# Kernel optimization log

Hardware: AMD Instinct MI355X
Metric: run time of the kernel (lower is better)

## Reference

```python
import jax, jax.numpy as jnp
import numpy as np

N_NODES = 100_000
N_EDGES = 1_600_000
D_FEAT = 128
D_HID = 128
D_OUT = 1


def _w(key, fan_in, fan_out):
    # PyG Linear default (glorot-ish); exact init irrelevant for a math reference
    return jax.random.normal(key, (fan_in, fan_out), dtype=jnp.float32) * (1.0 / np.sqrt(fan_in))


def setup_inputs() -> dict:
    key = jax.random.key(0)
    ks = jax.random.split(key, 20)
    inp = {
        "x": jax.random.normal(ks[0], (N_NODES, D_FEAT), dtype=jnp.float32),
        "edge_index": jax.random.randint(ks[1], (2, N_EDGES), 0, N_NODES, dtype=jnp.int32),
    }
    dims = [(D_FEAT, D_HID), (D_HID, D_HID), (D_HID, D_OUT)]
    i = 2
    for li, (din, dout) in enumerate(dims, start=1):
        inp[f"Wk{li}"] = _w(ks[i + 0], din, dout)
        inp[f"Wq{li}"] = _w(ks[i + 1], din, dout)
        inp[f"Wv{li}"] = _w(ks[i + 2], din, dout)
        inp[f"Ws{li}"] = _w(ks[i + 3], din, dout)
        inp[f"b{li}"] = jnp.zeros((dout,), dtype=jnp.float32)
        i += 4
    return inp


def _res_gated_conv(x, src, dst, Wk, Wq, Wv, Ws, b):
    # out_i = Ws x_i + b + sum_{j->i} sigmoid(Wk x_i + Wq x_j) * (Wv x_j)
    k = x @ Wk          # [N, Dout] (keyed by target)
    q = x @ Wq          # [N, Dout] (keyed by source)
    v = x @ Wv          # [N, Dout]
    eta = jax.nn.sigmoid(k[dst] + q[src])          # [E, Dout] edge gate
    msg = eta * v[src]                             # [E, Dout]
    agg = jax.ops.segment_sum(msg, dst, num_segments=x.shape[0])  # scatter-add
    return agg + x @ Ws + b


def reference(x, edge_index, Wk1, Wq1, Wv1, Ws1, b1, Wk2, Wq2, Wv2, Ws2, b2,
              Wk3, Wq3, Wv3, Ws3, b3):
    src = edge_index[0]
    dst = edge_index[1]
    x = jax.nn.relu(_res_gated_conv(x, src, dst, Wk1, Wq1, Wv1, Ws1, b1))
    x = jax.nn.relu(_res_gated_conv(x, src, dst, Wk2, Wq2, Wv2, Ws2, b2))
    return _res_gated_conv(x, src, dst, Wk3, Wq3, Wv3, Ws3, b3)  # [N, 1]
```

## Files before the change

kernel.cpp:

```cpp
#include <hip/hip_runtime.h>
#include <hip/hip_bf16.h>
#include <cstdint>

typedef unsigned short u16;
typedef unsigned int   u32;
typedef __attribute__((ext_vector_type(8))) short bf16x8;
typedef __attribute__((ext_vector_type(4))) float f32x4;

#define NEG_LOG2E -1.44269504088896f

__device__ __forceinline__ float bf2f(u16 u) {
    union { u32 i; float f; } c; c.i = ((u32)u) << 16; return c.f;
}
__device__ __forceinline__ u16 f2bf(float f) {
    union { float f; u32 i; } c; c.f = f;
    u32 x = c.i;
    return (u16)((x + 0x7fffu + ((x >> 16) & 1u)) >> 16);
}
__device__ __forceinline__ void bfu2(u32 p, float& lo, float& hi) {
    union { u32 i; float f; } a, b;
    a.i = p << 16; b.i = p & 0xffff0000u;
    lo = a.f; hi = b.f;
}
__device__ __forceinline__ float gate(float zt) {
    return __builtin_amdgcn_rcpf(1.0f + __builtin_amdgcn_exp2f(zt));
}

struct P8 { const float* p[8]; };
__global__ __launch_bounds__(256)
void prep_k(P8 wsrc, u16* __restrict__ Wt) {
    int t = threadIdx.x;
    int mat = blockIdx.x >> 3, seg = blockIdx.x & 7;
    const float* W = wsrc.p[mat];
    u16* T = Wt + (size_t)mat * 16384;
    for (int p = 0; p < 8; ++p) {
        int idx = seg * 2048 + p * 256 + t;
        int k = idx >> 7, n = idx & 127;
        T[n * 128 + k] = f2bf(W[k * 128 + n]);
    }
}


#define CSR_CH 2048

__global__ __launch_bounds__(256)
void sortA_hist(const int* __restrict__ dst, int* __restrict__ cnt,
                int nE, int NA, int nbuck) {
    __shared__ int lh[512];
    int t = threadIdx.x, b = blockIdx.x;
    for (int i = t; i < nbuck; i += 256) lh[i] = 0;
    __syncthreads();
    int i0 = b * CSR_CH, iend = min(i0 + CSR_CH, nE);
    for (int i = i0 + t; i < iend; i += 256) atomicAdd(&lh[dst[i] >> 8], 1);
    __syncthreads();
    for (int i = t; i < nbuck; i += 256) cnt[i * NA + b] = lh[i];
}

__global__ __launch_bounds__(256)
void scan_part_k(const int* __restrict__ arr, int* __restrict__ part, int M) {
    __shared__ int wsum[4];
    int t = threadIdx.x, lane = t & 63, wave = t >> 6;
    int i0 = blockIdx.x * 1024 + t * 4;
    int s = 0;
    for (int j = 0; j < 4; ++j) { int i = i0 + j; if (i < M) s += arr[i]; }
    for (int off = 32; off > 0; off >>= 1) s += __shfl_xor(s, off);
    if (lane == 0) wsum[wave] = s;
    __syncthreads();
    if (t == 0) part[blockIdx.x] = wsum[0] + wsum[1] + wsum[2] + wsum[3];
}

__global__ __launch_bounds__(512)
void scan_tops512(int* __restrict__ part, int nb) {
    __shared__ int sh[512];
    int t = threadIdx.x;
    int v = (t < nb) ? part[t] : 0;
    sh[t] = v;
    __syncthreads();
    for (int off = 1; off < 512; off <<= 1) {
        int u = (t >= off) ? sh[t - off] : 0;
        __syncthreads();
        sh[t] += u;
        __syncthreads();
    }
    if (t < nb) part[t] = sh[t] - v;
}

__global__ __launch_bounds__(256)
void scan_emit_k(const int* __restrict__ arr, const int* __restrict__ part,
                 int* __restrict__ outp, int M, int total) {
    __shared__ int woff[4];
    int t = threadIdx.x, lane = t & 63, wave = t >> 6;
    int i0 = blockIdx.x * 1024 + t * 4;
    int d[4]; int s = 0;
    for (int j = 0; j < 4; ++j) { int i = i0 + j; d[j] = (i < M) ? arr[i] : 0; s += d[j]; }
    int ws = s;
    for (int off = 1; off < 64; off <<= 1) {
        int u = __shfl_up(ws, off);
        if (lane >= off) ws += u;
    }
    if (lane == 63) woff[wave] = ws;
    __syncthreads();
    int base = part[blockIdx.x];
    for (int w = 0; w < wave; ++w) base += woff[w];
    int ex = base + ws - s;
    for (int j = 0; j < 4; ++j) {
        int i = i0 + j;
        if (i < M) outp[i] = ex;
        ex += d[j];
    }
    if (blockIdx.x == 0 && t == 0) outp[M] = total;
}

__global__ __launch_bounds__(256)
void sortA_scat(const int* __restrict__ src, const int* __restrict__ dst,
                const int* __restrict__ scnt, u32* __restrict__ tkey,
                int nE, int NA, int nbuck) {
    __shared__ int lh[512];
    __shared__ int lbase[512];
    int t = threadIdx.x, b = blockIdx.x;
    for (int i = t; i < nbuck; i += 256) { lh[i] = 0; lbase[i] = scnt[i * NA + b]; }
    __syncthreads();
    int i0 = b * CSR_CH, iend = min(i0 + CSR_CH, nE);
    for (int i = i0 + t; i < iend; i += 256) {
        int d = dst[i], s = src[i];
        int bk = d >> 8;
        int r = atomicAdd(&lh[bk], 1);
        tkey[lbase[bk] + r] = ((u32)(d & 255) << 24) | (u32)s;
    }
}

__global__ __launch_bounds__(256)
void sortB(const u32* __restrict__ tkey, const int* __restrict__ scnt,
           int* __restrict__ rowp, int* __restrict__ ssrc,
           int NA, int N, int nE) {
    __shared__ int h[256];
    __shared__ int off[256];
    int t = threadIdx.x, b = blockIdx.x;
    int base = scnt[b * NA];
    int endp = scnt[(b + 1) * NA];
    h[t] = 0;
    __syncthreads();
    for (int i = base + t; i < endp; i += 256)
        atomicAdd(&h[tkey[i] >> 24], 1);
    __syncthreads();
    int v = h[t];
    off[t] = v;
    __syncthreads();
    for (int d = 1; d < 256; d <<= 1) {
        int u = (t >= d) ? off[t - d] : 0;
        __syncthreads();
        off[t] += u;
        __syncthreads();
    }
    int ex = off[t] - v;
    __syncthreads();
    off[t] = ex;
    h[t] = 0;
    __syncthreads();
    int dglob = b * 256 + t;
    if (dglob < N) rowp[dglob] = base + ex;
    if (b == 0 && t == 0) rowp[N] = nE;
    for (int i = base + t; i < endp; i += 256) {
        u32 k = tkey[i];
        int loc = k >> 24;
        int r = atomicAdd(&h[loc], 1);
        ssrc[base + off[loc] + r] = (int)(k & 0xFFFFFFu);
    }
}

#define XS 136
template<int F32>
__global__ __launch_bounds__(256, 2)
void gemm_kqvs(const void* __restrict__ Xv, const u16* __restrict__ Wt,
               const float* __restrict__ bias,
               u16* __restrict__ KS, u16* __restrict__ QV, int nrows)
{
    __shared__ u16 xs[128 * XS];
    __shared__ u16 wsl[128 * XS];
    const int tid  = threadIdx.x;
    const int wave = tid >> 6, lane = tid & 63;
    const int quad = lane >> 4, l16 = lane & 15;
    const int r0 = blockIdx.x * 128;

    for (int p = 0; p < 8; ++p) {
        int c = p * 256 + tid;
        int row = c >> 4;
        int col = (c & 15) * 8;
        int gr = r0 + row; if (gr >= nrows) gr = nrows - 1;
        if (F32) {
            const float* sp = (const float*)Xv + (size_t)gr * 128 + col;
            float4 f0 = *(const float4*)(sp);
            float4 f1 = *(const float4*)(sp + 4);
            uint4 st;
            st.x = ((u32)f2bf(f0.y) << 16) | f2bf(f0.x);
            st.y = ((u32)f2bf(f0.w) << 16) | f2bf(f0.z);
            st.z = ((u32)f2bf(f1.y) << 16) | f2bf(f1.x);
            st.w = ((u32)f2bf(f1.w) << 16) | f2bf(f1.z);
            *(uint4*)(&xs[row * XS + col]) = st;
        } else {
            uint4 d = *(const uint4*)((const u16*)Xv + (size_t)gr * 128 + col);
            *(uint4*)(&xs[row * XS + col]) = d;
        }
    }

    for (int wi = 0; wi < 4; ++wi) {
        __syncthreads();
        const u16* Wsrc = Wt + wi * (128 * 128);
        for (int p = 0; p < 8; ++p) {
            int c = p * 256 + tid;
            int row = c >> 4;
            int col = (c & 15) * 8;
            uint4 d = *(const uint4*)(Wsrc + row * 128 + col);
            *(uint4*)(&wsl[row * XS + col]) = d;
        }
        __syncthreads();

        f32x4 acc[2][8];
        for (int mt = 0; mt < 2; ++mt)
            for (int nt = 0; nt < 8; ++nt) acc[mt][nt] = (f32x4)0.0f;

        const int cbase = wave * 32;
        for (int kt = 0; kt < 4; ++kt) {
            bf16x8 a0 = *(const bf16x8*)&wsl[(cbase + l16)      * XS + kt * 32 + quad * 8];
            bf16x8 a1 = *(const bf16x8*)&wsl[(cbase + 16 + l16) * XS + kt * 32 + quad * 8];
            for (int nt = 0; nt < 8; ++nt) {
                bf16x8 b = *(const bf16x8*)&xs[(nt * 16 + l16) * XS + kt * 32 + quad * 8];
                acc[0][nt] = __builtin_amdgcn_mfma_f32_16x16x32_bf16(a0, b, acc[0][nt], 0, 0, 0);
                acc[1][nt] = __builtin_amdgcn_mfma_f32_16x16x32_bf16(a1, b, acc[1][nt], 0, 0, 0);
            }
        }

        float4 bias4[2];
        if (wi == 3) {
            bias4[0] = *(const float4*)(bias + cbase + quad * 4);
            bias4[1] = *(const float4*)(bias + cbase + 16 + quad * 4);
        }
        for (int mt = 0; mt < 2; ++mt) {
            int chb = cbase + mt * 16 + quad * 4;
            for (int nt = 0; nt < 8; ++nt) {
                int node = r0 + nt * 16 + l16;
                if (node >= nrows) continue;
                f32x4 v = acc[mt][nt];
                float x0 = v[0], x1 = v[1], x2 = v[2], x3 = v[3];
                if (wi == 0 || wi == 1) {
                    x0 *= NEG_LOG2E; x1 *= NEG_LOG2E; x2 *= NEG_LOG2E; x3 *= NEG_LOG2E;
                } else if (wi == 3) {
                    x0 += bias4[mt].x; x1 += bias4[mt].y;
                    x2 += bias4[mt].z; x3 += bias4[mt].w;
                }
                uint2 st;
                st.x = ((u32)f2bf(x1) << 16) | f2bf(x0);
                st.y = ((u32)f2bf(x3) << 16) | f2bf(x2);
                size_t nb = (size_t)node * 256;
                if      (wi == 0) *(uint2*)(KS + nb + chb) = st;
                else if (wi == 3) *(uint2*)(KS + nb + 128 + chb) = st;
                else if (wi == 1) *(uint2*)(QV + nb + 2 * chb) = st;
                else              *(uint2*)(QV + nb + 2 * chb + 4) = st;
            }
        }
    }
}

template<int MODE>
__global__ __launch_bounds__(256)
void edge_csr2(const int* __restrict__ rowp, const int* __restrict__ ssrc,
               const u16* __restrict__ KS, const u16* __restrict__ QV,
               u16* __restrict__ Xout,
               const float* __restrict__ Wk3, const float* __restrict__ Wq3,
               const float* __restrict__ Wv3, const float* __restrict__ Ws3,
               const float* __restrict__ b3,
               float* __restrict__ k3, float2* __restrict__ qv3,
               float* __restrict__ s3, int N)
{
    const int lane = threadIdx.x & 63;
    const int half = lane >> 5;
    const int t    = lane & 31;
    int gw = blockIdx.x * (blockDim.x >> 6) + (threadIdx.x >> 6);
    int nw = gridDim.x * (blockDim.x >> 6);

    float4 wk4, wq4, wv4, ws4;
    float bias3 = 0.0f;
    if (MODE == 1) {
        wk4 = *(const float4*)(Wk3 + 4 * t);
        wq4 = *(const float4*)(Wq3 + 4 * t);
        wv4 = *(const float4*)(Wv3 + 4 * t);
        ws4 = *(const float4*)(Ws3 + 4 * t);
        bias3 = b3[0];
    }

#define LOAD2(S0, S1) (*((const uint4*)(QV + (size_t)(half ? (S1) : (S0)) * 256) + t))
#define COMP(QVv, A0, A1, A2, A3)                                             \
    {                                                                         \
        float q0_, q1_, q2_, q3_, v0_, v1_, v2_, v3_;                         \
        bfu2((QVv).x, q0_, q1_); bfu2((QVv).y, q2_, q3_);                     \
        bfu2((QVv).z, v0_, v1_); bfu2((QVv).w, v2_, v3_);                     \
        A0 += gate(k0 + q0_) * v0_;  A1 += gate(k1 + q1_) * v1_;              \
        A2 += gate(k2 + q2_) * v2_;  A3 += gate(k3v + q3_) * v3_;             \
    }

    for (int d = gw; d < N; d += nw) {
        int beg = rowp[d], end = rowp[d + 1];
        uint2 kk = *(const uint2*)(KS + (size_t)d * 256 + t * 4);
        float k0, k1, k2, k3v;
        bfu2(kk.x, k0, k1); bfu2(kk.y, k2, k3v);
        float a0 = 0.f, a1 = 0.f, a2 = 0.f, a3 = 0.f;
        float e0 = 0.f, e1 = 0.f, e2 = 0.f, e3 = 0.f;

        for (int base = beg; base < end; base += 64) {
            int e = base + lane;
            int sv = (e < end) ? ssrc[e] : 0;
            int m = end - base; if (m > 64) m = 64;
            int j = 0;
            for (; j + 4 <= m; j += 4) {
                int sa0 = __builtin_amdgcn_readlane(sv, j);
                int sa1 = __builtin_amdgcn_readlane(sv, j + 1);
                int sb0 = __builtin_amdgcn_readlane(sv, j + 2);
                int sb1 = __builtin_amdgcn_readlane(sv, j + 3);
                uint4 qA = LOAD2(sa0, sa1);
                uint4 qB = LOAD2(sb0, sb1);
                COMP(qA, a0, a1, a2, a3);
                COMP(qB, e0, e1, e2, e3);
            }
            if (j + 2 <= m) {
                int s0 = __builtin_amdgcn_readlane(sv, j);
                int s1 = __builtin_amdgcn_readlane(sv, j + 1);
                uint4 qA = LOAD2(s0, s1);
                COMP(qA, a0, a1, a2, a3);
                j += 2;
            }
            if (j < m) {
                int s0i = __builtin_amdgcn_readlane(sv, j);
                uint4 qv_ = *((const uint4*)(QV + (size_t)s0i * 256) + t);
                float q0_, q1_, q2_, q3_, v0_, v1_, v2_, v3_;
                bfu2(qv_.x, q0_, q1_); bfu2(qv_.y, q2_, q3_);
                bfu2(qv_.z, v0_, v1_); bfu2(qv_.w, v2_, v3_);
                if (half == 0) {
                    a0 += gate(k0 + q0_) * v0_;  a1 += gate(k1 + q1_) * v1_;
                    a2 += gate(k2 + q2_) * v2_;  a3 += gate(k3v + q3_) * v3_;
                }
            }
        }
#undef LOAD2
#undef COMP

        a0 += e0; a1 += e1; a2 += e2; a3 += e3;
        a0 += __shfl_xor(a0, 32);
        a1 += __shfl_xor(a1, 32);
        a2 += __shfl_xor(a2, 32);
        a3 += __shfl_xor(a3, 32);

        uint2 ss = *(const uint2*)(KS + (size_t)d * 256 + 128 + t * 4);
        float s0f, s1f, s2f, s3f;
        bfu2(ss.x, s0f, s1f); bfu2(ss.y, s2f, s3f);
        float r0 = fmaxf(s0f + a0, 0.f);
        float r1 = fmaxf(s1f + a1, 0.f);
        float r2 = fmaxf(s2f + a2, 0.f);
        float r3 = fmaxf(s3f + a3, 0.f);

        if (MODE == 0) {
            if (half == 0) {
                uint2 st;
                st.x = ((u32)f2bf(r1) << 16) | f2bf(r0);
                st.y = ((u32)f2bf(r3) << 16) | f2bf(r2);
                *(uint2*)(Xout + (size_t)d * 128 + t * 4) = st;
            }
        } else {
            float pk = r0 * wk4.x + r1 * wk4.y + r2 * wk4.z + r3 * wk4.w;
            float pq = r0 * wq4.x + r1 * wq4.y + r2 * wq4.z + r3 * wq4.w;
            float pv = r0 * wv4.x + r1 * wv4.y + r2 * wv4.z + r3 * wv4.w;
            float ps = r0 * ws4.x + r1 * ws4.y + r2 * ws4.z + r3 * ws4.w;
            for (int off = 1; off < 32; off <<= 1) {
                pk += __shfl_xor(pk, off);
                pq += __shfl_xor(pq, off);
                pv += __shfl_xor(pv, off);
                ps += __shfl_xor(ps, off);
            }
            if (lane == 0) {
                k3[d]  = NEG_LOG2E * pk;
                qv3[d] = make_float2(NEG_LOG2E * pq, pv);
                s3[d]  = ps + bias3;
            }
        }
    }
}

__global__ __launch_bounds__(256)
void edge3_csr(const int* __restrict__ rowp, const int* __restrict__ ssrc,
               const float* __restrict__ k3, const float2* __restrict__ qv3,
               const float* __restrict__ s3, float* __restrict__ outp, int N)
{
    int lane = threadIdx.x & 63;
    int gw = blockIdx.x * (blockDim.x >> 6) + (threadIdx.x >> 6);
    int nw = gridDim.x * (blockDim.x >> 6);
    for (int d = gw; d < N; d += nw) {
        int beg = rowp[d], end = rowp[d + 1];
        float kd = k3[d];
        float sum = 0.0f;
        for (int e = beg + lane; e < end; e += 64) {
            float2 qv = qv3[ssrc[e]];
            sum += gate(kd + qv.x) * qv.y;
        }
        for (int off = 32; off > 0; off >>= 1) sum += __shfl_xor(sum, off);
        if (lane == 0) outp[d] = s3[d] + sum;
    }
}

extern "C" void kernel_launch(void* const* d_in, const int* in_sizes, int n_in,
                              void* d_out, int out_size, void* d_ws, size_t ws_size,
                              hipStream_t stream)
{
    const float* x0 = (const float*)d_in[0];
    const int*   ei = (const int*)d_in[1];
    const int    N  = in_sizes[0] / 128;
    const int    E  = in_sizes[1] / 2;
    const int* src = ei;
    const int* dst = ei + E;

    const int NBUCK = (N + 255) >> 8;
    const int NA    = (E + CSR_CH - 1) / CSR_CH;
    const int M     = NBUCK * NA;
    const int nparts = (M + 1023) / 1024;

    char* ws = (char*)d_ws;
    size_t off = 0;
    auto carve = [&](size_t bytes) { void* p = ws + off; off += (bytes + 255) & ~(size_t)255; return p; };
    u16*    Wt   = (u16*)carve((size_t)8 * 16384 * sizeof(u16));
    u16*    bufX = (u16*)carve((size_t)N * 128 * sizeof(u16));
    u16*    KS   = (u16*)carve((size_t)N * 256 * sizeof(u16));
    u16*    QV   = (u16*)carve((size_t)N * 256 * sizeof(u16));
    int*    ssrc = (int*)carve((size_t)E * sizeof(int));
    u32*    tkey = (u32*)carve((size_t)E * sizeof(u32));
    int*    rowp = (int*)carve((size_t)(N + 1) * sizeof(int));
    int*    cnt  = (int*)carve((size_t)M * sizeof(int));
    int*    scnt = (int*)carve((size_t)(M + 1) * sizeof(int));
    int*    part = (int*)carve((size_t)512 * sizeof(int));
    float*  k3   = (float*)carve((size_t)N * sizeof(float));
    float2* qv3  = (float2*)carve((size_t)N * sizeof(float2));
    float*  s3   = (float*)carve((size_t)N * sizeof(float));

    P8 wp;
    wp.p[0] = (const float*)d_in[2];  wp.p[1] = (const float*)d_in[3];
    wp.p[2] = (const float*)d_in[4];  wp.p[3] = (const float*)d_in[5];
    wp.p[4] = (const float*)d_in[7];  wp.p[5] = (const float*)d_in[8];
    wp.p[6] = (const float*)d_in[9];  wp.p[7] = (const float*)d_in[10];
    prep_k<<<64, 256, 0, stream>>>(wp, Wt);

    sortA_hist<<<NA, 256, 0, stream>>>(dst, cnt, E, NA, NBUCK);
    scan_part_k<<<nparts, 256, 0, stream>>>(cnt, part, M);
    scan_tops512<<<1, 512, 0, stream>>>(part, nparts);
    scan_emit_k<<<nparts, 256, 0, stream>>>(cnt, part, scnt, M, E);
    sortA_scat<<<NA, 256, 0, stream>>>(src, dst, scnt, tkey, E, NA, NBUCK);
    sortB<<<NBUCK, 256, 0, stream>>>(tkey, scnt, rowp, ssrc, NA, N, E);

    int gb = (N + 127) / 128;

    gemm_kqvs<1><<<gb, 256, 0, stream>>>(x0, Wt, (const float*)d_in[6], KS, QV, N);
    edge_csr2<0><<<4096, 256, 0, stream>>>(rowp, ssrc, KS, QV, bufX,
        nullptr, nullptr, nullptr, nullptr, nullptr, nullptr, nullptr, nullptr, N);
    gemm_kqvs<0><<<gb, 256, 0, stream>>>(bufX, Wt + 4 * 16384, (const float*)d_in[11], KS, QV, N);
    edge_csr2<1><<<4096, 256, 0, stream>>>(rowp, ssrc, KS, QV, nullptr,
        (const float*)d_in[12], (const float*)d_in[13], (const float*)d_in[14],
        (const float*)d_in[15], (const float*)d_in[16],
        k3, qv3, s3, N);
    edge3_csr<<<2048, 256, 0, stream>>>(rowp, ssrc, k3, qv3, s3, (float*)d_out, N);
}
```

Measured before the change: 554.6 us.

## Merge independent setup kernels into shared launches to cut launch count

Folds the weight transpose into the histogram kernel, merges the top-level partial scan into each emit block, and runs the CSR bucket sort alongside the first-layer GEMM in a single launch by splitting on block index. This removes three kernel launches and their inter-kernel gaps. In exchange, every emit block now redundantly scans all partials, and the sort blocks inherit the GEMM's large shared-memory allocation, which can limit how many blocks fit per CU.

Result: faster. 541.4 us (-2.4%).

```diff
diff --git a/kernel.cpp b/kernel.cpp
--- a/kernel.cpp
+++ b/kernel.cpp
@@ -26,34 +26,34 @@
     return __builtin_amdgcn_rcpf(1.0f + __builtin_amdgcn_exp2f(zt));
 }
 
+#define CSR_CH 2048
+#define XS 136
+
 struct P8 { const float* p[8]; };
 __global__ __launch_bounds__(256)
-void prep_k(P8 wsrc, u16* __restrict__ Wt) {
+void prep_hist_k(P8 wsrc, u16* __restrict__ Wt,
+                 const int* __restrict__ dst, int* __restrict__ cnt,
+                 int nE, int NA, int nbuck) {
+    __shared__ int lh[512];
     int t = threadIdx.x;
-    int mat = blockIdx.x >> 3, seg = blockIdx.x & 7;
-    const float* W = wsrc.p[mat];
-    u16* T = Wt + (size_t)mat * 16384;
-    for (int p = 0; p < 8; ++p) {
-        int idx = seg * 2048 + p * 256 + t;
-        int k = idx >> 7, n = idx & 127;
-        T[n * 128 + k] = f2bf(W[k * 128 + n]);
-    }
-}
-
-
-#define CSR_CH 2048
-
-__global__ __launch_bounds__(256)
-void sortA_hist(const int* __restrict__ dst, int* __restrict__ cnt,
-                int nE, int NA, int nbuck) {
-    __shared__ int lh[512];
-    int t = threadIdx.x, b = blockIdx.x;
-    for (int i = t; i < nbuck; i += 256) lh[i] = 0;
-    __syncthreads();
-    int i0 = b * CSR_CH, iend = min(i0 + CSR_CH, nE);
-    for (int i = i0 + t; i < iend; i += 256) atomicAdd(&lh[dst[i] >> 8], 1);
-    __syncthreads();
-    for (int i = t; i < nbuck; i += 256) cnt[i * NA + b] = lh[i];
+    if (blockIdx.x < 64) {
+        int mat = blockIdx.x >> 3, seg = blockIdx.x & 7;
+        const float* W = wsrc.p[mat];
+        u16* T = Wt + (size_t)mat * 16384;
+        for (int p = 0; p < 8; ++p) {
+            int idx = seg * 2048 + p * 256 + t;
+            int k = idx >> 7, n = idx & 127;
+            T[n * 128 + k] = f2bf(W[k * 128 + n]);
+        }
+    } else {
+        int b = blockIdx.x - 64;
+        for (int i = t; i < nbuck; i += 256) lh[i] = 0;
+        __syncthreads();
+        int i0 = b * CSR_CH, iend = min(i0 + CSR_CH, nE);
+        for (int i = i0 + t; i < iend; i += 256) atomicAdd(&lh[dst[i] >> 8], 1);
+        __syncthreads();
+        for (int i = t; i < nbuck; i += 256) cnt[i * NA + b] = lh[i];
+    }
 }
 
 __global__ __launch_bounds__(256)
@@ -69,27 +69,25 @@
     if (t == 0) part[blockIdx.x] = wsum[0] + wsum[1] + wsum[2] + wsum[3];
 }
 
-__global__ __launch_bounds__(512)
-void scan_tops512(int* __restrict__ part, int nb) {
+__global__ __launch_bounds__(256)
+void scan_emit2_k(const int* __restrict__ arr, const int* __restrict__ part,
+                  int* __restrict__ outp, int M, int total, int nparts) {
     __shared__ int sh[512];
-    int t = threadIdx.x;
-    int v = (t < nb) ? part[t] : 0;
-    sh[t] = v;
-    __syncthreads();
-    for (int off = 1; off < 512; off <<= 1) {
-        int u = (t >= off) ? sh[t - off] : 0;
-        __syncthreads();
-        sh[t] += u;
-        __syncthreads();
-    }
-    if (t < nb) part[t] = sh[t] - v;
-}
-
-__global__ __launch_bounds__(256)
-void scan_emit_k(const int* __restrict__ arr, const int* __restrict__ part,
-                 int* __restrict__ outp, int M, int total) {
     __shared__ int woff[4];
     int t = threadIdx.x, lane = t & 63, wave = t >> 6;
+    sh[t]       = (t < nparts)       ? part[t]       : 0;
+    sh[t + 256] = (t + 256 < nparts) ? part[t + 256] : 0;
+    __syncthreads();
+    for (int off = 1; off < 512; off <<= 1) {
+        int u0 = (t >= off)       ? sh[t - off]       : 0;
+        int u1 = (t + 256 >= off) ? sh[t + 256 - off] : 0;
+        __syncthreads();
+        sh[t] += u0; sh[t + 256] += u1;
+        __syncthreads();
+    }
+    int base = (blockIdx.x == 0) ? 0 : sh[blockIdx.x - 1];
+    __syncthreads();
+
     int i0 = blockIdx.x * 1024 + t * 4;
     int d[4]; int s = 0;
     for (int j = 0; j < 4; ++j) { int i = i0 + j; d[j] = (i < M) ? arr[i] : 0; s += d[j]; }
@@ -100,7 +98,6 @@
     }
     if (lane == 63) woff[wave] = ws;
     __syncthreads();
-    int base = part[blockIdx.x];
     for (int w = 0; w < wave; ++w) base += woff[w];
     int ex = base + ws - s;
     for (int j = 0; j < 4; ++j) {
@@ -129,13 +126,11 @@
     }
 }
 
-__global__ __launch_bounds__(256)
-void sortB(const u32* __restrict__ tkey, const int* __restrict__ scnt,
-           int* __restrict__ rowp, int* __restrict__ ssrc,
-           int NA, int N, int nE) {
-    __shared__ int h[256];
-    __shared__ int off[256];
-    int t = threadIdx.x, b = blockIdx.x;
+__device__ __forceinline__
+void sortB_body(const u32* __restrict__ tkey, const int* __restrict__ scnt,
+                int* __restrict__ rowp, int* __restrict__ ssrc,
+                int NA, int N, int nE, int b, int* h, int* offv) {
+    int t = threadIdx.x;
     int base = scnt[b * NA];
     int endp = scnt[(b + 1) * NA];
     h[t] = 0;
@@ -144,17 +139,17 @@
         atomicAdd(&h[tkey[i] >> 24], 1);
     __syncthreads();
     int v = h[t];
-    off[t] = v;
+    offv[t] = v;
     __syncthreads();
     for (int d = 1; d < 256; d <<= 1) {
-        int u = (t >= d) ? off[t - d] : 0;
-        __syncthreads();
-        off[t] += u;
-        __syncthreads();
-    }
-    int ex = off[t] - v;
-    __syncthreads();
-    off[t] = ex;
+        int u = (t >= d) ? offv[t - d] : 0;
+        __syncthreads();
+        offv[t] += u;
+        __syncthreads();
+    }
+    int ex = offv[t] - v;
+    __syncthreads();
+    offv[t] = ex;
     h[t] = 0;
     __syncthreads();
     int dglob = b * 256 + t;
@@ -164,23 +159,21 @@
         u32 k = tkey[i];
         int loc = k >> 24;
         int r = atomicAdd(&h[loc], 1);
-        ssrc[base + off[loc] + r] = (int)(k & 0xFFFFFFu);
-    }
-}
-
-#define XS 136
+        ssrc[base + offv[loc] + r] = (int)(k & 0xFFFFFFu);
+    }
+}
+
 template<int F32>
-__global__ __launch_bounds__(256, 2)
-void gemm_kqvs(const void* __restrict__ Xv, const u16* __restrict__ Wt,
+__device__ __forceinline__
+void gemm_body(int bid, u16* xs, u16* wsl,
+               const void* __restrict__ Xv, const u16* __restrict__ Wt,
                const float* __restrict__ bias,
                u16* __restrict__ KS, u16* __restrict__ QV, int nrows)
 {
-    __shared__ u16 xs[128 * XS];
-    __shared__ u16 wsl[128 * XS];
     const int tid  = threadIdx.x;
     const int wave = tid >> 6, lane = tid & 63;
     const int quad = lane >> 4, l16 = lane & 15;
-    const int r0 = blockIdx.x * 128;
+    const int r0 = bid * 128;
 
     for (int p = 0; p < 8; ++p) {
         int c = p * 256 + tid;
@@ -261,6 +254,35 @@
     }
 }
 
+__global__ __launch_bounds__(256, 2)
+void sortB_gemm1(const u32* __restrict__ tkey, const int* __restrict__ scnt,
+                 int* __restrict__ rowp, int* __restrict__ ssrc,
+                 int NA, int N, int nE, int nbuck,
+                 const float* __restrict__ x0, const u16* __restrict__ Wt,
+                 const float* __restrict__ bias,
+                 u16* __restrict__ KS, u16* __restrict__ QV)
+{
+    __shared__ u16 xs[128 * XS];
+    __shared__ u16 wsl[128 * XS];
+    if ((int)blockIdx.x < nbuck) {
+        int* h = (int*)xs;
+        int* offv = h + 256;
+        sortB_body(tkey, scnt, rowp, ssrc, NA, N, nE, blockIdx.x, h, offv);
+    } else {
+        gemm_body<1>(blockIdx.x - nbuck, xs, wsl, x0, Wt, bias, KS, QV, N);
+    }
+}
+
+__global__ __launch_bounds__(256, 2)
+void gemm_l2(const u16* __restrict__ X, const u16* __restrict__ Wt,
+             const float* __restrict__ bias,
+             u16* __restrict__ KS, u16* __restrict__ QV, int nrows)
+{
+    __shared__ u16 xs[128 * XS];
+    __shared__ u16 wsl[128 * XS];
+    gemm_body<0>(blockIdx.x, xs, wsl, X, Wt, bias, KS, QV, nrows);
+}
+
 template<int MODE>
 __global__ __launch_bounds__(256)
 void edge_csr2(const int* __restrict__ rowp, const int* __restrict__ ssrc,
@@ -443,21 +465,18 @@
     wp.p[2] = (const float*)d_in[4];  wp.p[3] = (const float*)d_in[5];
     wp.p[4] = (const float*)d_in[7];  wp.p[5] = (const float*)d_in[8];
     wp.p[6] = (const float*)d_in[9];  wp.p[7] = (const float*)d_in[10];
-    prep_k<<<64, 256, 0, stream>>>(wp, Wt);
-
-    sortA_hist<<<NA, 256, 0, stream>>>(dst, cnt, E, NA, NBUCK);
+
+    int gb = (N + 127) / 128;
+
+    prep_hist_k<<<64 + NA, 256, 0, stream>>>(wp, Wt, dst, cnt, E, NA, NBUCK);
     scan_part_k<<<nparts, 256, 0, stream>>>(cnt, part, M);
-    scan_tops512<<<1, 512, 0, stream>>>(part, nparts);
-    scan_emit_k<<<nparts, 256, 0, stream>>>(cnt, part, scnt, M, E);
+    scan_emit2_k<<<nparts, 256, 0, stream>>>(cnt, part, scnt, M, E, nparts);
     sortA_scat<<<NA, 256, 0, stream>>>(src, dst, scnt, tkey, E, NA, NBUCK);
-    sortB<<<NBUCK, 256, 0, stream>>>(tkey, scnt, rowp, ssrc, NA, N, E);
-
-    int gb = (N + 127) / 128;
-
-    gemm_kqvs<1><<<gb, 256, 0, stream>>>(x0, Wt, (const float*)d_in[6], KS, QV, N);
+    sortB_gemm1<<<NBUCK + gb, 256, 0, stream>>>(tkey, scnt, rowp, ssrc, NA, N, E, NBUCK,
+        x0, Wt, (const float*)d_in[6], KS, QV);
     edge_csr2<0><<<4096, 256, 0, stream>>>(rowp, ssrc, KS, QV, bufX,
         nullptr, nullptr, nullptr, nullptr, nullptr, nullptr, nullptr, nullptr, N);
-    gemm_kqvs<0><<<gb, 256, 0, stream>>>(bufX, Wt + 4 * 16384, (const float*)d_in[11], KS, QV, N);
+    gemm_l2<<<gb, 256, 0, stream>>>(bufX, Wt + 4 * 16384, (const float*)d_in[11], KS, QV, N);
     edge_csr2<1><<<4096, 256, 0, stream>>>(rowp, ssrc, KS, QV, nullptr,
         (const float*)d_in[12], (const float*)d_in[13], (const float*)d_in[14],
         (const float*)d_in[15], (const float*)d_in[16],
```
